# Performance work log

Hardware: AMD Instinct MI355X
Metric: run time of the kernel (lower is better)

The kernel has to match this reference:

```python
import jax, jax.numpy as jnp
import numpy as np

VARIATION_SCALE = 0.05
TEMPORAL_SMOOTHING = 0.9
TEMPERATURE = 1.0
N_PATTERNS = 8


def setup_inputs() -> dict:
    key = jax.random.key(0)
    k_x, k_w, k_p, k_n = jax.random.split(key, 4)
    B, T, H = 4, 8192, 1024
    return {
        "x": jax.random.normal(k_x, (B, T, H), jnp.float32),
        "W_sel": jax.random.normal(k_w, (H, N_PATTERNS), jnp.float32) * 0.02,
        "b_sel": jnp.zeros((N_PATTERNS,), jnp.float32),
        "patterns": jax.random.normal(k_p, (N_PATTERNS, H), jnp.float32) * 0.1,
        "noise": jax.random.normal(k_n, (B, T, H), jnp.float32),
    }


def reference(x, W_sel, b_sel, patterns, noise):
    # pattern mixture: softmax over 8 learned patterns, per token
    logits = (jnp.einsum("bth,hp->btp", x, W_sel) + b_sel) * TEMPERATURE  # [B,T,8]
    pattern_weights = jax.nn.softmax(logits, axis=-1)
    variation = jnp.einsum("btp,ph->bth", pattern_weights, patterns)  # [B,T,H]

    # EMA noise recurrence: state_t = s*state_{t-1} + (1-s)*eps_t, state_0 = 0
    eps = noise * (VARIATION_SCALE * TEMPERATURE)  # [B,T,H]

    def step(carry, e_t):
        c = TEMPORAL_SMOOTHING * carry + (1.0 - TEMPORAL_SMOOTHING) * e_t
        return c, c

    init = jnp.zeros((x.shape[0], x.shape[2]), x.dtype)  # [B,H]
    _, states = jax.lax.scan(step, init, jnp.swapaxes(eps, 0, 1))  # [T,B,H]
    states = jnp.swapaxes(states, 0, 1)  # [B,T,H]

    return x + variation + states
```

## Files before the change

### kernel.cpp

```cpp
#include <hip/hip_runtime.h>


#define T_LEN 8192
#define H_DIM 1024
#define B_DIM 4
#define NPAT 8
#define CHUNK 64
#define WARM 64
#define NCHUNK (T_LEN / CHUNK)
#define HSPLIT 4
#define HSL (H_DIM / HSPLIT)

static_assert(WARM <= CHUNK, "warm-up must stay within previous chunk");

__global__ __launch_bounds__(256) void kA_weights(
    const float* __restrict__ x, const float* __restrict__ Wsel,
    const float* __restrict__ bsel, float* __restrict__ wts)
{
    const int wave = threadIdx.x >> 6;
    const int lane = threadIdx.x & 63;
    const int tok0 = blockIdx.x * 32 + wave * 8;

    float a[64];
#pragma unroll
    for (int q = 0; q < 64; ++q) a[q] = 0.0f;

    const float* xbase = x + (size_t)tok0 * H_DIM + lane;

#pragma unroll 2
    for (int r = 0; r < 16; ++r) {
        const int h = r * 64 + lane;
        const float4 wa = *(const float4*)(Wsel + (size_t)h * NPAT);
        const float4 wb = *(const float4*)(Wsel + (size_t)h * NPAT + 4);
        float xv[8];
#pragma unroll
        for (int j = 0; j < 8; ++j)
            xv[j] = xbase[(size_t)j * H_DIM + r * 64];
#pragma unroll
        for (int j = 0; j < 8; ++j) {
            a[j * 8 + 0] = fmaf(xv[j], wa.x, a[j * 8 + 0]);
            a[j * 8 + 1] = fmaf(xv[j], wa.y, a[j * 8 + 1]);
            a[j * 8 + 2] = fmaf(xv[j], wa.z, a[j * 8 + 2]);
            a[j * 8 + 3] = fmaf(xv[j], wa.w, a[j * 8 + 3]);
            a[j * 8 + 4] = fmaf(xv[j], wb.x, a[j * 8 + 4]);
            a[j * 8 + 5] = fmaf(xv[j], wb.y, a[j * 8 + 5]);
            a[j * 8 + 6] = fmaf(xv[j], wb.z, a[j * 8 + 6]);
            a[j * 8 + 7] = fmaf(xv[j], wb.w, a[j * 8 + 7]);
        }
    }

#pragma unroll
    for (int s = 0; s < 6; ++s) {
        const int o = 1 << s;
        const int half = 32 >> s;
        const bool hib = (lane & o) != 0;
#pragma unroll
        for (int m = 0; m < half; ++m) {
            const float lo = a[2 * m];
            const float hi = a[2 * m + 1];
            const float disc = hib ? lo : hi;
            const float keep = hib ? hi : lo;
            a[m] = keep + __shfl_xor(disc, o, 64);
        }
    }

    const float logit = a[0] + bsel[lane & 7];

    float mx = logit;
    mx = fmaxf(mx, __shfl_xor(mx, 1, 64));
    mx = fmaxf(mx, __shfl_xor(mx, 2, 64));
    mx = fmaxf(mx, __shfl_xor(mx, 4, 64));
    const float e = __expf(logit - mx);
    float sum = e;
    sum += __shfl_xor(sum, 1, 64);
    sum += __shfl_xor(sum, 2, 64);
    sum += __shfl_xor(sum, 4, 64);

    wts[(size_t)tok0 * NPAT + lane] = e / sum;
}

__global__ __launch_bounds__(256) void kB_fused(
    const float* __restrict__ x, const float* __restrict__ noise,
    const float* __restrict__ patterns, const float* __restrict__ wts,
    float* __restrict__ out)
{
    __shared__ float wsm[CHUNK * NPAT];

    const int cid = blockIdx.x;
    const int hs  = cid & (HSPLIT - 1);
    const int bc  = cid >> 2;
    const int b   = bc >> 7;
    const int c   = bc & (NCHUNK - 1);
    const int t0  = c * CHUNK;
    const size_t tokbase = (size_t)b * T_LEN + t0;
    const int tid = threadIdx.x;
    const int h   = hs * HSL + tid;

    *(float2*)(wsm + tid * 2) = *(const float2*)(wts + tokbase * NPAT + tid * 2);
    __syncthreads();

    float pat[NPAT];
#pragma unroll
    for (int p = 0; p < NPAT; ++p)
        pat[p] = patterns[p * H_DIM + h];

    float s = 0.0f;
    const int nw = (c == 0) ? 0 : WARM;
    const float* nptr = noise + (tokbase - nw) * (size_t)H_DIM + h;
#pragma unroll 8
    for (int i = 0; i < nw; ++i) {
        s = fmaf(0.9f, s, 0.005f * (*nptr));
        nptr += H_DIM;
    }

    const float* xptr = x + tokbase * H_DIM + h;
    float*       optr = out + tokbase * H_DIM + h;
#pragma unroll 8
    for (int i = 0; i < CHUNK; ++i) {
        const float nv = *nptr;
        const float xv = *xptr;
        s = fmaf(0.9f, s, 0.005f * nv);

        const float4 wA = *(const float4*)(wsm + i * NPAT);
        const float4 wB = *(const float4*)(wsm + i * NPAT + 4);
        float v = 0.0f;
        v = fmaf(wA.x, pat[0], v);
        v = fmaf(wA.y, pat[1], v);
        v = fmaf(wA.z, pat[2], v);
        v = fmaf(wA.w, pat[3], v);
        v = fmaf(wB.x, pat[4], v);
        v = fmaf(wB.y, pat[5], v);
        v = fmaf(wB.z, pat[6], v);
        v = fmaf(wB.w, pat[7], v);

        *optr = xv + v + s;
        nptr += H_DIM; xptr += H_DIM; optr += H_DIM;
    }
}

extern "C" void kernel_launch(void* const* d_in, const int* in_sizes, int n_in,
                              void* d_out, int out_size, void* d_ws, size_t ws_size,
                              hipStream_t stream) {
    const float* x        = (const float*)d_in[0];
    const float* Wsel     = (const float*)d_in[1];
    const float* bsel     = (const float*)d_in[2];
    const float* patterns = (const float*)d_in[3];
    const float* noise    = (const float*)d_in[4];
    float* out = (float*)d_out;
    float* wts = (float*)d_ws;

    const int n_tok = B_DIM * T_LEN;
    kA_weights<<<n_tok / 32, 256, 0, stream>>>(x, Wsel, bsel, wts);
    kB_fused<<<B_DIM * NCHUNK * HSPLIT, 256, 0, stream>>>(x, noise, patterns, wts, out);
}
```

Baseline: 376.3 us.

## Fuse softmax weight computation into the EMA/output kernel with block-wide reduction

Merges the pattern-weight kernel into the main streaming kernel. Each 1024-thread block covers all of H for a 128-token chunk and computes logits via in-wave shuffle reductions plus a shared-memory cross-wave sum. This removes the second read of x and the workspace round-trip. The larger chunk also halves the relative cost of the noise warm-up. In exchange it adds per-sub-step barriers, high register pressure, and fewer, larger blocks.

```diff
diff --git a/kernel.cpp b/kernel.cpp
--- a/kernel.cpp
+++ b/kernel.cpp
@@ -5,104 +5,36 @@
 #define H_DIM 1024
 #define B_DIM 4
 #define NPAT 8
-#define CHUNK 64
+#define CHUNK 128
+#define SUB 8
+#define NSUB (CHUNK / SUB)
 #define WARM 64
 #define NCHUNK (T_LEN / CHUNK)
-#define HSPLIT 4
-#define HSL (H_DIM / HSPLIT)
+#define RSTR 17
 
 static_assert(WARM <= CHUNK, "warm-up must stay within previous chunk");
 
-__global__ __launch_bounds__(256) void kA_weights(
-    const float* __restrict__ x, const float* __restrict__ Wsel,
-    const float* __restrict__ bsel, float* __restrict__ wts)
+__global__ __launch_bounds__(1024, 4) void kF_fused(
+    const float* __restrict__ x, const float* __restrict__ noise,
+    const float* __restrict__ Wsel, const float* __restrict__ bsel,
+    const float* __restrict__ patterns, float* __restrict__ out)
 {
-    const int wave = threadIdx.x >> 6;
-    const int lane = threadIdx.x & 63;
-    const int tok0 = blockIdx.x * 32 + wave * 8;
+    __shared__ float red[2][64 * RSTR];
 
-    float a[64];
-#pragma unroll
-    for (int q = 0; q < 64; ++q) a[q] = 0.0f;
+    const int tid  = threadIdx.x;
+    const int wave = tid >> 6;
+    const int lane = tid & 63;
+    const int b    = blockIdx.x >> 6;
+    const int c    = blockIdx.x & (NCHUNK - 1);
+    const size_t tokbase = (size_t)b * T_LEN + c * CHUNK;
+    const int h    = tid;
 
-    const float* xbase = x + (size_t)tok0 * H_DIM + lane;
-
-#pragma unroll 2
-    for (int r = 0; r < 16; ++r) {
-        const int h = r * 64 + lane;
-        const float4 wa = *(const float4*)(Wsel + (size_t)h * NPAT);
-        const float4 wb = *(const float4*)(Wsel + (size_t)h * NPAT + 4);
-        float xv[8];
-#pragma unroll
-        for (int j = 0; j < 8; ++j)
-            xv[j] = xbase[(size_t)j * H_DIM + r * 64];
-#pragma unroll
-        for (int j = 0; j < 8; ++j) {
-            a[j * 8 + 0] = fmaf(xv[j], wa.x, a[j * 8 + 0]);
-            a[j * 8 + 1] = fmaf(xv[j], wa.y, a[j * 8 + 1]);
-            a[j * 8 + 2] = fmaf(xv[j], wa.z, a[j * 8 + 2]);
-            a[j * 8 + 3] = fmaf(xv[j], wa.w, a[j * 8 + 3]);
-            a[j * 8 + 4] = fmaf(xv[j], wb.x, a[j * 8 + 4]);
-            a[j * 8 + 5] = fmaf(xv[j], wb.y, a[j * 8 + 5]);
-            a[j * 8 + 6] = fmaf(xv[j], wb.z, a[j * 8 + 6]);
-            a[j * 8 + 7] = fmaf(xv[j], wb.w, a[j * 8 + 7]);
-        }
-    }
-
-#pragma unroll
-    for (int s = 0; s < 6; ++s) {
-        const int o = 1 << s;
-        const int half = 32 >> s;
-        const bool hib = (lane & o) != 0;
-#pragma unroll
-        for (int m = 0; m < half; ++m) {
-            const float lo = a[2 * m];
-            const float hi = a[2 * m + 1];
-            const float disc = hib ? lo : hi;
-            const float keep = hib ? hi : lo;
-            a[m] = keep + __shfl_xor(disc, o, 64);
-        }
-    }
-
-    const float logit = a[0] + bsel[lane & 7];
-
-    float mx = logit;
-    mx = fmaxf(mx, __shfl_xor(mx, 1, 64));
-    mx = fmaxf(mx, __shfl_xor(mx, 2, 64));
-    mx = fmaxf(mx, __shfl_xor(mx, 4, 64));
-    const float e = __expf(logit - mx);
-    float sum = e;
-    sum += __shfl_xor(sum, 1, 64);
-    sum += __shfl_xor(sum, 2, 64);
-    sum += __shfl_xor(sum, 4, 64);
-
-    wts[(size_t)tok0 * NPAT + lane] = e / sum;
-}
-
-__global__ __launch_bounds__(256) void kB_fused(
-    const float* __restrict__ x, const float* __restrict__ noise,
-    const float* __restrict__ patterns, const float* __restrict__ wts,
-    float* __restrict__ out)
-{
-    __shared__ float wsm[CHUNK * NPAT];
-
-    const int cid = blockIdx.x;
-    const int hs  = cid & (HSPLIT - 1);
-    const int bc  = cid >> 2;
-    const int b   = bc >> 7;
-    const int c   = bc & (NCHUNK - 1);
-    const int t0  = c * CHUNK;
-    const size_t tokbase = (size_t)b * T_LEN + t0;
-    const int tid = threadIdx.x;
-    const int h   = hs * HSL + tid;
-
-    *(float2*)(wsm + tid * 2) = *(const float2*)(wts + tokbase * NPAT + tid * 2);
-    __syncthreads();
-
+    const float4 wa = *(const float4*)(Wsel + (size_t)h * NPAT);
+    const float4 wb = *(const float4*)(Wsel + (size_t)h * NPAT + 4);
     float pat[NPAT];
 #pragma unroll
-    for (int p = 0; p < NPAT; ++p)
-        pat[p] = patterns[p * H_DIM + h];
+    for (int p = 0; p < NPAT; ++p) pat[p] = patterns[p * H_DIM + h];
+    const float bs = bsel[lane & 7];
 
     float s = 0.0f;
     const int nw = (c == 0) ? 0 : WARM;
@@ -113,28 +45,104 @@
         nptr += H_DIM;
     }
 
-    const float* xptr = x + tokbase * H_DIM + h;
+    const float* xld = x + tokbase * H_DIM + h;
     float*       optr = out + tokbase * H_DIM + h;
-#pragma unroll 8
-    for (int i = 0; i < CHUNK; ++i) {
-        const float nv = *nptr;
-        const float xv = *xptr;
-        s = fmaf(0.9f, s, 0.005f * nv);
 
-        const float4 wA = *(const float4*)(wsm + i * NPAT);
-        const float4 wB = *(const float4*)(wsm + i * NPAT + 4);
-        float v = 0.0f;
-        v = fmaf(wA.x, pat[0], v);
-        v = fmaf(wA.y, pat[1], v);
-        v = fmaf(wA.z, pat[2], v);
-        v = fmaf(wA.w, pat[3], v);
-        v = fmaf(wB.x, pat[4], v);
-        v = fmaf(wB.y, pat[5], v);
-        v = fmaf(wB.z, pat[6], v);
-        v = fmaf(wB.w, pat[7], v);
+    float xc[SUB];
+#pragma unroll
+    for (int j = 0; j < SUB; ++j)
+        xc[j] = xld[(size_t)j * H_DIM];
+    xld += (size_t)SUB * H_DIM;
 
-        *optr = xv + v + s;
-        nptr += H_DIM; xptr += H_DIM; optr += H_DIM;
+    for (int st = 0; st < NSUB; ++st) {
+        const int buf = st & 1;
+
+        float a[64];
+#pragma unroll
+        for (int j = 0; j < SUB; ++j) {
+            a[j * 8 + 0] = xc[j] * wa.x;
+            a[j * 8 + 1] = xc[j] * wa.y;
+            a[j * 8 + 2] = xc[j] * wa.z;
+            a[j * 8 + 3] = xc[j] * wa.w;
+            a[j * 8 + 4] = xc[j] * wb.x;
+            a[j * 8 + 5] = xc[j] * wb.y;
+            a[j * 8 + 6] = xc[j] * wb.z;
+            a[j * 8 + 7] = xc[j] * wb.w;
+        }
+#pragma unroll
+        for (int sp = 0; sp < 6; ++sp) {
+            const int o = 1 << sp;
+            const int half = 32 >> sp;
+            const bool hib = (lane & o) != 0;
+#pragma unroll
+            for (int m = 0; m < half; ++m) {
+                const float lo = a[2 * m];
+                const float hi = a[2 * m + 1];
+                const float disc = hib ? lo : hi;
+                const float keep = hib ? hi : lo;
+                a[m] = keep + __shfl_xor(disc, o, 64);
+            }
+        }
+        red[buf][lane * RSTR + wave] = a[0];
+
+        float xn[SUB];
+        if (st + 1 < NSUB) {
+#pragma unroll
+            for (int j = 0; j < SUB; ++j)
+                xn[j] = xld[(size_t)j * H_DIM];
+            xld += (size_t)SUB * H_DIM;
+        }
+
+        __syncthreads();
+
+        float tot = 0.0f;
+#pragma unroll
+        for (int w = 0; w < 16; ++w)
+            tot += red[buf][lane * RSTR + w];
+        const float logit = tot + bs;
+
+        float mx = logit;
+        mx = fmaxf(mx, __shfl_xor(mx, 1, 64));
+        mx = fmaxf(mx, __shfl_xor(mx, 2, 64));
+        mx = fmaxf(mx, __shfl_xor(mx, 4, 64));
+        const float e = __expf(logit - mx);
+        float den = e;
+        den += __shfl_xor(den, 1, 64);
+        den += __shfl_xor(den, 2, 64);
+        den += __shfl_xor(den, 4, 64);
+        const float wgt = e / den;
+
+#pragma unroll
+        for (int j = 0; j < SUB; ++j) {
+            const float w0 = __shfl(wgt, j * 8 + 0, 64);
+            const float w1 = __shfl(wgt, j * 8 + 1, 64);
+            const float w2 = __shfl(wgt, j * 8 + 2, 64);
+            const float w3 = __shfl(wgt, j * 8 + 3, 64);
+            const float w4 = __shfl(wgt, j * 8 + 4, 64);
+            const float w5 = __shfl(wgt, j * 8 + 5, 64);
+            const float w6 = __shfl(wgt, j * 8 + 6, 64);
+            const float w7 = __shfl(wgt, j * 8 + 7, 64);
+
+            const float nv = *nptr;
+            s = fmaf(0.9f, s, 0.005f * nv);
+
+            float v = 0.0f;
+            v = fmaf(w0, pat[0], v);
+            v = fmaf(w1, pat[1], v);
+            v = fmaf(w2, pat[2], v);
+            v = fmaf(w3, pat[3], v);
+            v = fmaf(w4, pat[4], v);
+            v = fmaf(w5, pat[5], v);
+            v = fmaf(w6, pat[6], v);
+            v = fmaf(w7, pat[7], v);
+
+            *optr = xc[j] + v + s;
+            nptr += H_DIM;
+            optr += H_DIM;
+        }
+
+#pragma unroll
+        for (int j = 0; j < SUB; ++j) xc[j] = xn[j];
     }
 }
 
@@ -147,9 +155,8 @@
     const float* patterns = (const float*)d_in[3];
     const float* noise    = (const float*)d_in[4];
     float* out = (float*)d_out;
-    float* wts = (float*)d_ws;
+    (void)d_ws; (void)ws_size;
 
-    const int n_tok = B_DIM * T_LEN;
-    kA_weights<<<n_tok / 32, 256, 0, stream>>>(x, Wsel, bsel, wts);
-    kB_fused<<<B_DIM * NCHUNK * HSPLIT, 256, 0, stream>>>(x, noise, patterns, wts, out);
+    kF_fused<<<B_DIM * NCHUNK, 1024, 0, stream>>>(x, noise, Wsel, bsel,
+                                                  patterns, out);
 }
```

After: 358.1 us. 4.8% less time.

## Fuse softmax weight computation into streaming kernel with larger chunks

Applied to the files above, without the earlier changes.

Merges the logits/softmax kernel into the main EMA+mixture kernel. Each 1024-thread block now computes its own 128 tokens' pattern weights into shared memory before streaming the full hidden dimension. This removes the workspace round trip and a second launch. It also gives x a chance to be re-read from cache, and the larger chunk halves the relative cost of the noise warm-up. The risk is low occupancy: one large block per CU with a 64-register accumulator array, and no overlap between the logit phase and the streaming phase.

```diff
diff --git a/kernel.cpp b/kernel.cpp
--- a/kernel.cpp
+++ b/kernel.cpp
@@ -5,104 +5,26 @@
 #define H_DIM 1024
 #define B_DIM 4
 #define NPAT 8
-#define CHUNK 64
+#define CHUNK 128
 #define WARM 64
 #define NCHUNK (T_LEN / CHUNK)
-#define HSPLIT 4
-#define HSL (H_DIM / HSPLIT)
 
 static_assert(WARM <= CHUNK, "warm-up must stay within previous chunk");
 
-__global__ __launch_bounds__(256) void kA_weights(
-    const float* __restrict__ x, const float* __restrict__ Wsel,
-    const float* __restrict__ bsel, float* __restrict__ wts)
-{
-    const int wave = threadIdx.x >> 6;
-    const int lane = threadIdx.x & 63;
-    const int tok0 = blockIdx.x * 32 + wave * 8;
-
-    float a[64];
-#pragma unroll
-    for (int q = 0; q < 64; ++q) a[q] = 0.0f;
-
-    const float* xbase = x + (size_t)tok0 * H_DIM + lane;
-
-#pragma unroll 2
-    for (int r = 0; r < 16; ++r) {
-        const int h = r * 64 + lane;
-        const float4 wa = *(const float4*)(Wsel + (size_t)h * NPAT);
-        const float4 wb = *(const float4*)(Wsel + (size_t)h * NPAT + 4);
-        float xv[8];
-#pragma unroll
-        for (int j = 0; j < 8; ++j)
-            xv[j] = xbase[(size_t)j * H_DIM + r * 64];
-#pragma unroll
-        for (int j = 0; j < 8; ++j) {
-            a[j * 8 + 0] = fmaf(xv[j], wa.x, a[j * 8 + 0]);
-            a[j * 8 + 1] = fmaf(xv[j], wa.y, a[j * 8 + 1]);
-            a[j * 8 + 2] = fmaf(xv[j], wa.z, a[j * 8 + 2]);
-            a[j * 8 + 3] = fmaf(xv[j], wa.w, a[j * 8 + 3]);
-            a[j * 8 + 4] = fmaf(xv[j], wb.x, a[j * 8 + 4]);
-            a[j * 8 + 5] = fmaf(xv[j], wb.y, a[j * 8 + 5]);
-            a[j * 8 + 6] = fmaf(xv[j], wb.z, a[j * 8 + 6]);
-            a[j * 8 + 7] = fmaf(xv[j], wb.w, a[j * 8 + 7]);
-        }
-    }
-
-#pragma unroll
-    for (int s = 0; s < 6; ++s) {
-        const int o = 1 << s;
-        const int half = 32 >> s;
-        const bool hib = (lane & o) != 0;
-#pragma unroll
-        for (int m = 0; m < half; ++m) {
-            const float lo = a[2 * m];
-            const float hi = a[2 * m + 1];
-            const float disc = hib ? lo : hi;
-            const float keep = hib ? hi : lo;
-            a[m] = keep + __shfl_xor(disc, o, 64);
-        }
-    }
-
-    const float logit = a[0] + bsel[lane & 7];
-
-    float mx = logit;
-    mx = fmaxf(mx, __shfl_xor(mx, 1, 64));
-    mx = fmaxf(mx, __shfl_xor(mx, 2, 64));
-    mx = fmaxf(mx, __shfl_xor(mx, 4, 64));
-    const float e = __expf(logit - mx);
-    float sum = e;
-    sum += __shfl_xor(sum, 1, 64);
-    sum += __shfl_xor(sum, 2, 64);
-    sum += __shfl_xor(sum, 4, 64);
-
-    wts[(size_t)tok0 * NPAT + lane] = e / sum;
-}
-
-__global__ __launch_bounds__(256) void kB_fused(
+__global__ __launch_bounds__(1024, 4) void kF_fused(
     const float* __restrict__ x, const float* __restrict__ noise,
-    const float* __restrict__ patterns, const float* __restrict__ wts,
-    float* __restrict__ out)
+    const float* __restrict__ Wsel, const float* __restrict__ bsel,
+    const float* __restrict__ patterns, float* __restrict__ out)
 {
     __shared__ float wsm[CHUNK * NPAT];
 
-    const int cid = blockIdx.x;
-    const int hs  = cid & (HSPLIT - 1);
-    const int bc  = cid >> 2;
-    const int b   = bc >> 7;
-    const int c   = bc & (NCHUNK - 1);
-    const int t0  = c * CHUNK;
-    const size_t tokbase = (size_t)b * T_LEN + t0;
-    const int tid = threadIdx.x;
-    const int h   = hs * HSL + tid;
-
-    *(float2*)(wsm + tid * 2) = *(const float2*)(wts + tokbase * NPAT + tid * 2);
-    __syncthreads();
-
-    float pat[NPAT];
-#pragma unroll
-    for (int p = 0; p < NPAT; ++p)
-        pat[p] = patterns[p * H_DIM + h];
+    const int tid  = threadIdx.x;
+    const int wave = tid >> 6;
+    const int lane = tid & 63;
+    const int b    = blockIdx.x >> 6;
+    const int c    = blockIdx.x & (NCHUNK - 1);
+    const size_t tokbase = (size_t)b * T_LEN + c * CHUNK;
+    const int h    = tid;
 
     float s = 0.0f;
     const int nw = (c == 0) ? 0 : WARM;
@@ -112,6 +34,71 @@
         s = fmaf(0.9f, s, 0.005f * (*nptr));
         nptr += H_DIM;
     }
+
+    float pat[NPAT];
+#pragma unroll
+    for (int p = 0; p < NPAT; ++p) pat[p] = patterns[p * H_DIM + h];
+
+    {
+        float a[64];
+#pragma unroll
+        for (int q = 0; q < 64; ++q) a[q] = 0.0f;
+
+        const float* xw = x + (tokbase + (size_t)wave * 8) * H_DIM + lane;
+
+#pragma unroll 2
+        for (int r = 0; r < 16; ++r) {
+            const int hh = r * 64 + lane;
+            const float4 wa = *(const float4*)(Wsel + (size_t)hh * NPAT);
+            const float4 wb = *(const float4*)(Wsel + (size_t)hh * NPAT + 4);
+            float xv[8];
+#pragma unroll
+            for (int j = 0; j < 8; ++j)
+                xv[j] = xw[(size_t)j * H_DIM + r * 64];
+#pragma unroll
+            for (int j = 0; j < 8; ++j) {
+                a[j * 8 + 0] = fmaf(xv[j], wa.x, a[j * 8 + 0]);
+                a[j * 8 + 1] = fmaf(xv[j], wa.y, a[j * 8 + 1]);
+                a[j * 8 + 2] = fmaf(xv[j], wa.z, a[j * 8 + 2]);
+                a[j * 8 + 3] = fmaf(xv[j], wa.w, a[j * 8 + 3]);
+                a[j * 8 + 4] = fmaf(xv[j], wb.x, a[j * 8 + 4]);
+                a[j * 8 + 5] = fmaf(xv[j], wb.y, a[j * 8 + 5]);
+                a[j * 8 + 6] = fmaf(xv[j], wb.z, a[j * 8 + 6]);
+                a[j * 8 + 7] = fmaf(xv[j], wb.w, a[j * 8 + 7]);
+            }
+        }
+
+#pragma unroll
+        for (int sp = 0; sp < 6; ++sp) {
+            const int o = 1 << sp;
+            const int half = 32 >> sp;
+            const bool hib = (lane & o) != 0;
+#pragma unroll
+            for (int m = 0; m < half; ++m) {
+                const float lo = a[2 * m];
+                const float hi = a[2 * m + 1];
+                const float disc = hib ? lo : hi;
+                const float keep = hib ? hi : lo;
+                a[m] = keep + __shfl_xor(disc, o, 64);
+            }
+        }
+
+        const float logit = a[0] + bsel[lane & 7];
+
+        float mx = logit;
+        mx = fmaxf(mx, __shfl_xor(mx, 1, 64));
+        mx = fmaxf(mx, __shfl_xor(mx, 2, 64));
+        mx = fmaxf(mx, __shfl_xor(mx, 4, 64));
+        const float e = __expf(logit - mx);
+        float den = e;
+        den += __shfl_xor(den, 1, 64);
+        den += __shfl_xor(den, 2, 64);
+        den += __shfl_xor(den, 4, 64);
+
+        wsm[wave * 64 + lane] = e / den;
+    }
+
+    __syncthreads();
 
     const float* xptr = x + tokbase * H_DIM + h;
     float*       optr = out + tokbase * H_DIM + h;
@@ -147,9 +134,8 @@
     const float* patterns = (const float*)d_in[3];
     const float* noise    = (const float*)d_in[4];
     float* out = (float*)d_out;
-    float* wts = (float*)d_ws;
+    (void)d_ws; (void)ws_size;
 
-    const int n_tok = B_DIM * T_LEN;
-    kA_weights<<<n_tok / 32, 256, 0, stream>>>(x, Wsel, bsel, wts);
-    kB_fused<<<B_DIM * NCHUNK * HSPLIT, 256, 0, stream>>>(x, noise, patterns, wts, out);
+    kF_fused<<<B_DIM * NCHUNK, 1024, 0, stream>>>(x, noise, Wsel, bsel,
+                                                  patterns, out);
 }
```

New measurement: 360.8 us. -4.1%, faster.
